# Kernel tuning notes

Hardware: AMD Instinct MI355X
Metric: run time of the kernel (lower is better)

Reference implementation:

```python
import jax, jax.numpy as jnp
import numpy as np

B, LATENT = 8192, 1024
NR, NC = 12, 12                      # nb_rows, nb_cols
H0, W0 = NR + 2, NC + 2              # 14x14 after reshape
EPS = 1e-5
SLOPE = 0.01                         # LeakyReLU default


def setup_inputs() -> dict:
    key = jax.random.key(0)
    ks = jax.random.split(key, 9)
    s = 0.05
    return {
        "x": jax.random.normal(ks[0], (B, LATENT), jnp.float32),
        "fc_w": jax.random.normal(ks[1], (H0 * W0 * 36, LATENT), jnp.float32) * s,
        "fc_b": jax.random.normal(ks[2], (H0 * W0 * 36,), jnp.float32) * s,
        "conv_w": jax.random.normal(ks[3], (16, 36, 2, 2), jnp.float32) * s,
        "conv_b": jax.random.normal(ks[4], (16,), jnp.float32) * s,
        "gamma": jnp.ones((16,), jnp.float32),
        "beta": jnp.zeros((16,), jnp.float32),
        # locally-connected weights: (out_ch, in_ch, Hout, Wout, k*k)
        "lw1": jax.random.normal(ks[5], (6, 16, H0 - 1, W0 - 1, 4), jnp.float32) * s,
        "lw2": jax.random.normal(ks[6], (1, 6, H0 - 2, W0 - 2, 4), jnp.float32) * s,
    }


def _leaky(x):
    return jnp.where(x >= 0, x, SLOPE * x)


def _local_conv2(x, w):
    # x: (B,C,H,W); w: (O,C,Ho,Wo,4) with k=2, stride 1, no padding
    Ho, Wo = w.shape[2], w.shape[3]
    patches = jnp.stack(
        [x[:, :, dy:dy + Ho, dx:dx + Wo] for dy in (0, 1) for dx in (0, 1)],
        axis=-1)  # (B,C,Ho,Wo,4)
    return jnp.einsum('bchwk,ochwk->bohw', patches, w)


def reference(x, fc_w, fc_b, conv_w, conv_b, gamma, beta, lw1, lw2):
    # fc -> view(B, H0, W0, 36) -> permute to NCHW
    h = x @ fc_w.T + fc_b
    h = h.reshape(B, H0, W0, 36).transpose(0, 3, 1, 2)  # (B,36,14,14)
    # Conv2d k=2 padding='same' (torch pads bottom/right for even kernels)
    h = jax.lax.conv_general_dilated(
        h, conv_w, window_strides=(1, 1), padding=((0, 1), (0, 1)),
        dimension_numbers=('NCHW', 'OIHW', 'NCHW')) + conv_b[None, :, None, None]
    h = _leaky(h)
    # BatchNorm2d (training mode: batch stats, biased var)
    mu = h.mean(axis=(0, 2, 3), keepdims=True)
    var = h.var(axis=(0, 2, 3), keepdims=True)
    h = (h - mu) * jax.lax.rsqrt(var + EPS)
    h = h * gamma[None, :, None, None] + beta[None, :, None, None]
    # locally-connected stack: 14x14 -> 13x13 -> 12x12
    h = _leaky(_local_conv2(h, lw1))
    return _local_conv2(h, lw2)  # (B,1,12,12)
```

## Files before the change

### kernel.cpp

```cpp
#include <hip/hip_runtime.h>


#define SLOPE 0.01f

typedef __bf16 bf16x8 __attribute__((ext_vector_type(8)));
typedef float f32x4 __attribute__((ext_vector_type(4)));

typedef const __attribute__((address_space(1))) void* gas_ptr;
typedef __attribute__((address_space(3))) void* las_ptr;

__device__ __forceinline__ void load16_to_lds(const void* g, void* l) {
  __builtin_amdgcn_global_load_lds((gas_ptr)g, (las_ptr)l, 16, 0, 0);
}

__device__ __forceinline__ unsigned short f2bf(float f) {
  union { float f; unsigned int u; } v; v.f = f;
  unsigned int r = v.u + 0x7FFFu + ((v.u >> 16) & 1u);
  return (unsigned short)(r >> 16);
}
__device__ __forceinline__ float bfbits2f(unsigned int bits16) {
  union { unsigned int u; float f; } v; v.u = bits16 << 16;
  return v.f;
}
__device__ __forceinline__ float leaky(float v) { return v >= 0.f ? v : SLOPE * v; }

__global__ void k_cast_x(const float* __restrict__ x, unsigned short* __restrict__ xb,
                         float* __restrict__ stats) {
  if (blockIdx.x == 0 && threadIdx.x < 32) stats[threadIdx.x] = 0.f;
  int gid = blockIdx.x * 256 + threadIdx.x;
  const float4* x4 = (const float4*)x;
  float4 a = x4[gid * 2], b = x4[gid * 2 + 1];
  union { unsigned short s[8]; uint4 v; } o;
  o.s[0] = f2bf(a.x); o.s[1] = f2bf(a.y); o.s[2] = f2bf(a.z); o.s[3] = f2bf(a.w);
  o.s[4] = f2bf(b.x); o.s[5] = f2bf(b.y); o.s[6] = f2bf(b.z); o.s[7] = f2bf(b.w);
  ((uint4*)xb)[gid] = o.v;
}

__global__ void k_fold(const float* __restrict__ fc_w, const float* __restrict__ fc_b,
                       const float* __restrict__ conv_w, const float* __restrict__ conv_b,
                       unsigned short* __restrict__ Wc, float* __restrict__ bc) {
  __shared__ float cw[2304];
  int blk = blockIdx.x, og = blockIdx.y, t = threadIdx.x;
  if (blk == 196) {
    if (og != 0) return;
    uint4 z = make_uint4(0, 0, 0, 0);
    uint4* dst = (uint4*)(Wc + 3136 * 1024);
    for (int i = t; i < 24576; i += 256) dst[i] = z;
    for (int i = 3136 + t; i < 3328; i += 256) bc[i] = 0.f;
    return;
  }
  for (int i = t; i < 2304; i += 256) cw[i] = conv_w[i];
  __syncthreads();
  int i0 = blk / 14, j0 = blk - (blk / 14) * 14;
  float acc[4][4];
#pragma unroll
  for (int o = 0; o < 4; o++)
#pragma unroll
    for (int q = 0; q < 4; q++) acc[o][q] = 0.f;
  for (int c = 0; c < 36; c++) {
#pragma unroll
    for (int dy = 0; dy < 2; dy++) {
      int ii = i0 + dy; if (ii > 13) continue;
#pragma unroll
      for (int dx = 0; dx < 2; dx++) {
        int jj = j0 + dx; if (jj > 13) continue;
        int row = (ii * 14 + jj) * 36 + c;
        float4 f = *(const float4*)(fc_w + row * 1024 + t * 4);
        int kk = dy * 2 + dx;
#pragma unroll
        for (int oo = 0; oo < 4; oo++) {
          int o = og * 4 + oo;
          float w = cw[(o * 36 + c) * 4 + kk];
          acc[oo][0] += w * f.x; acc[oo][1] += w * f.y;
          acc[oo][2] += w * f.z; acc[oo][3] += w * f.w;
        }
      }
    }
  }
#pragma unroll
  for (int oo = 0; oo < 4; oo++) {
    int o = og * 4 + oo;
    int n = o * 196 + i0 * 14 + j0;
    union { unsigned short s[4]; uint2 v; } u;
    u.s[0] = f2bf(acc[oo][0]); u.s[1] = f2bf(acc[oo][1]);
    u.s[2] = f2bf(acc[oo][2]); u.s[3] = f2bf(acc[oo][3]);
    *(uint2*)(Wc + n * 1024 + t * 4) = u.v;
  }
  if (og == 0 && t < 16) {
    int o = t;
    float b = conv_b[o];
    for (int c = 0; c < 36; c++)
      for (int dy = 0; dy < 2; dy++) {
        int ii = i0 + dy; if (ii > 13) continue;
        for (int dx = 0; dx < 2; dx++) {
          int jj = j0 + dx; if (jj > 13) continue;
          b += cw[(o * 36 + c) * 4 + dy * 2 + dx] * fc_b[(ii * 14 + jj) * 36 + c];
        }
      }
    bc[o * 196 + i0 * 14 + j0] = b;
  }
}

__global__ __launch_bounds__(512, 1) void k_gemm(const unsigned short* __restrict__ Xb,
                                                 const unsigned short* __restrict__ Wcb,
                                                 const float* __restrict__ bc,
                                                 unsigned short* __restrict__ h2,
                                                 float* __restrict__ stats) {
  __shared__ __align__(16) char lds[32768];
  __shared__ float red[8][4];
  const int t = threadIdx.x;
  const int w = t >> 6, lane = t & 63;
  const int quad = lane >> 4, l15 = lane & 15;
  const int d = blockIdx.x;
  const int xcd = d & 7, j = d >> 3;
  const int mblk = xcd * 4 + (j & 3);
  const int nblk = j >> 2;
  const int m0 = mblk * 256, n0 = nblk * 256;
  const int mrow = t & 255, tko = t >> 8;
  const unsigned short* ga = Xb + (m0 + mrow) * 1024 + tko * 8;
  const unsigned short* gb = Wcb + (n0 + mrow) * 1024 + tko * 8;
  char* lA = lds;
  char* lB = lds + 16384;
  const int wm = w >> 2, wn = w & 3;
  const int wm0 = wm * 128, wn0 = wn * 64;

  f32x4 acc[8][4];
#pragma unroll
  for (int a = 0; a < 8; a++)
#pragma unroll
    for (int b = 0; b < 4; b++) acc[a][b] = (f32x4){0.f, 0.f, 0.f, 0.f};

  for (int kb = 0; kb < 1024; kb += 32) {
    __syncthreads();
    load16_to_lds(ga + kb,      lA + t * 16);
    load16_to_lds(ga + kb + 16, lA + 8192 + t * 16);
    load16_to_lds(gb + kb,      lB + t * 16);
    load16_to_lds(gb + kb + 16, lB + 8192 + t * 16);
    __syncthreads();

    bf16x8 af[8], bfr[4];
#pragma unroll
    for (int mb = 0; mb < 8; mb++)
      af[mb] = *(const bf16x8*)(lA + quad * 4096 + (wm0 + mb * 16 + l15) * 16);
#pragma unroll
    for (int nb = 0; nb < 4; nb++)
      bfr[nb] = *(const bf16x8*)(lB + quad * 4096 + (wn0 + nb * 16 + l15) * 16);
#pragma unroll
    for (int mb = 0; mb < 8; mb++)
#pragma unroll
      for (int nb = 0; nb < 4; nb++)
        acc[mb][nb] = __builtin_amdgcn_mfma_f32_16x16x32_bf16(af[mb], bfr[nb], acc[mb][nb], 0, 0, 0);
  }

  const int chLo = (n0 + wn0) / 196;
  float ss0 = 0.f, ss1 = 0.f, sq0 = 0.f, sq1 = 0.f;
#pragma unroll
  for (int nb = 0; nb < 4; nb++) {
    int colb = n0 + wn0 + nb * 16;
    int col = colb + l15;
    float bias = bc[col];
    bool store_ok = colb < 3200;
    bool cnt = colb < 3136;
    bool hi = (col / 196) != chLo;
    float cs = 0.f, cq = 0.f;
#pragma unroll
    for (int mb = 0; mb < 8; mb++) {
#pragma unroll
      for (int r = 0; r < 4; r++) {
        int row = m0 + wm0 + mb * 16 + quad * 4 + r;
        float v = leaky(acc[mb][nb][r] + bias);
        if (store_ok) h2[row * 3200 + col] = f2bf(v);
        cs += v; cq += v * v;
      }
    }
    if (cnt) {
      if (hi) { ss1 += cs; sq1 += cq; } else { ss0 += cs; sq0 += cq; }
    }
  }
#pragma unroll
  for (int off = 1; off < 64; off <<= 1) {
    ss0 += __shfl_xor(ss0, off, 64);
    ss1 += __shfl_xor(ss1, off, 64);
    sq0 += __shfl_xor(sq0, off, 64);
    sq1 += __shfl_xor(sq1, off, 64);
  }
  if (lane == 0) { red[w][0] = ss0; red[w][1] = ss1; red[w][2] = sq0; red[w][3] = sq1; }
  __syncthreads();
  if (t == 0) {
#pragma unroll
    for (int w2 = 0; w2 < 8; w2++) {
      int cl = (n0 + (w2 & 3) * 64) / 196;
      if (cl < 16) {
        atomicAdd(&stats[cl], red[w2][0]);
        atomicAdd(&stats[16 + cl], red[w2][2]);
      }
      if (cl + 1 < 16) {
        atomicAdd(&stats[cl + 1], red[w2][1]);
        atomicAdd(&stats[16 + cl + 1], red[w2][3]);
      }
    }
  }
}

__global__ __launch_bounds__(256) void k_tail(const unsigned short* __restrict__ h2,
                                              const float* __restrict__ stats,
                                              const float* __restrict__ gamma,
                                              const float* __restrict__ beta,
                                              const float* __restrict__ lw1,
                                              const float* __restrict__ lw2,
                                              float* __restrict__ out) {
  __shared__ unsigned short h3[4 * 3138];
  __shared__ float h4[4 * 1015];
  __shared__ float sc[16], sh[16];
  int b0 = blockIdx.x * 4, t = threadIdx.x;
  if (t < 16) {
    const float inv = 1.f / 1605632.f;
    float mean = stats[t] * inv;
    float var = stats[16 + t] * inv - mean * mean;
    float rstd = rsqrtf(var + 1e-5f);
    float s = gamma[t] * rstd;
    sc[t] = s; sh[t] = beta[t] - mean * s;
  }
  __syncthreads();
  for (int i = t; i < 6272; i += 256) {
    int bb = i / 1568, q = i - bb * 1568;
    int n = q * 2, o = n / 196;
    unsigned int u = *(const unsigned int*)(h2 + (b0 + bb) * 3200 + n);
    float v0 = bfbits2f(u & 0xffffu) * sc[o] + sh[o];
    float v1 = bfbits2f(u >> 16) * sc[o] + sh[o];
    unsigned int pk = (unsigned int)f2bf(v0) | ((unsigned int)f2bf(v1) << 16);
    *(unsigned int*)(h3 + bb * 3138 + n) = pk;
  }
  __syncthreads();
  for (int u = t; u < 312; u += 256) {
    int bb = u & 3, rest = u >> 2;
    int o = rest / 13, y = rest - o * 13;
    float acc[13];
#pragma unroll
    for (int x = 0; x < 13; x++) acc[x] = 0.f;
    const unsigned short* hb = h3 + bb * 3138;
    for (int c = 0; c < 16; c++) {
      float r0[14], r1[14];
      const unsigned int* p0 = (const unsigned int*)(hb + c * 196 + y * 14);
      const unsigned int* p1 = (const unsigned int*)(hb + c * 196 + (y + 1) * 14);
#pragma unroll
      for (int q = 0; q < 7; q++) {
        unsigned int v0 = p0[q], v1 = p1[q];
        r0[2 * q] = bfbits2f(v0 & 0xffffu); r0[2 * q + 1] = bfbits2f(v0 >> 16);
        r1[2 * q] = bfbits2f(v1 & 0xffffu); r1[2 * q + 1] = bfbits2f(v1 >> 16);
      }
      const float4* wp4 = (const float4*)(lw1 + (((o * 16 + c) * 13 + y) * 13) * 4);
#pragma unroll
      for (int x = 0; x < 13; x++) {
        float4 wv = wp4[x];
        acc[x] += r0[x] * wv.x + r0[x + 1] * wv.y +
                  r1[x] * wv.z + r1[x + 1] * wv.w;
      }
    }
#pragma unroll
    for (int x = 0; x < 13; x++)
      h4[bb * 1015 + (o * 13 + y) * 13 + x] = leaky(acc[x]);
  }
  __syncthreads();
  for (int oi = t; oi < 576; oi += 256) {
    int pos = oi >> 2, bb = oi & 3;
    int y = pos / 12, x = pos - y * 12;
    float a = 0.f;
    const float* hp = h4 + bb * 1015;
    const float4* w4 = (const float4*)lw2;
#pragma unroll
    for (int c = 0; c < 6; c++) {
      float4 wv = w4[(c * 12 + y) * 12 + x];
      int hb = c * 169 + y * 13 + x;
      a += hp[hb] * wv.x + hp[hb + 1] * wv.y +
           hp[hb + 13] * wv.z + hp[hb + 14] * wv.w;
    }
    out[(b0 + bb) * 144 + pos] = a;
  }
}

extern "C" void kernel_launch(void* const* d_in, const int* in_sizes, int n_in,
                              void* d_out, int out_size, void* d_ws, size_t ws_size,
                              hipStream_t stream) {
  const float* x      = (const float*)d_in[0];
  const float* fc_w   = (const float*)d_in[1];
  const float* fc_b   = (const float*)d_in[2];
  const float* conv_w = (const float*)d_in[3];
  const float* conv_b = (const float*)d_in[4];
  const float* gamma  = (const float*)d_in[5];
  const float* beta   = (const float*)d_in[6];
  const float* lw1    = (const float*)d_in[7];
  const float* lw2    = (const float*)d_in[8];

  char* ws = (char*)d_ws;
  unsigned short* Xb    = (unsigned short*)(ws);
  unsigned short* Wc    = (unsigned short*)(ws + 16777216);
  float*          bc    = (float*)(ws + 23592960);
  float*          stats = (float*)(ws + 23606272);
  unsigned short* h2    = (unsigned short*)(ws + 23606400);

  k_cast_x<<<4096, 256, 0, stream>>>(x, Xb, stats);
  k_fold<<<dim3(197, 4), 256, 0, stream>>>(fc_w, fc_b, conv_w, conv_b, Wc, bc);
  k_gemm<<<416, 512, 0, stream>>>(Xb, Wc, bc, h2, stats);
  k_tail<<<2048, 256, 0, stream>>>(h2, stats, gamma, beta, lw1, lw2, (float*)d_out);
}
```

Measured before the change: 431.9 us.

## Double-buffer GEMM K-loop, reorganize weight folding, and share weights across rows in local conv

The bf16 GEMM now uses two 64-wide K stages in a 128KB LDS double buffer. The next stage is issued before computing the current one, which halves the barriers per K and overlaps global loads with MFMA. The weight-folding kernel now gives each thread one K column and all 16 output channels, with grid y split over K instead of output groups, which changes its memory access pattern. The first locally-connected layer now has each thread process two batch rows so each weight load is reused twice, at the cost of fewer active threads and more registers.

```diff
diff --git a/kernel.cpp b/kernel.cpp
--- a/kernel.cpp
+++ b/kernel.cpp
@@ -40,9 +40,9 @@
                        const float* __restrict__ conv_w, const float* __restrict__ conv_b,
                        unsigned short* __restrict__ Wc, float* __restrict__ bc) {
   __shared__ float cw[2304];
-  int blk = blockIdx.x, og = blockIdx.y, t = threadIdx.x;
+  int blk = blockIdx.x, kg = blockIdx.y, t = threadIdx.x;
   if (blk == 196) {
-    if (og != 0) return;
+    if (kg != 0) return;
     uint4 z = make_uint4(0, 0, 0, 0);
     uint4* dst = (uint4*)(Wc + 3136 * 1024);
     for (int i = t; i < 24576; i += 256) dst[i] = z;
@@ -52,11 +52,10 @@
   for (int i = t; i < 2304; i += 256) cw[i] = conv_w[i];
   __syncthreads();
   int i0 = blk / 14, j0 = blk - (blk / 14) * 14;
-  float acc[4][4];
-#pragma unroll
-  for (int o = 0; o < 4; o++)
-#pragma unroll
-    for (int q = 0; q < 4; q++) acc[o][q] = 0.f;
+  int kcol = kg * 256 + t;
+  float acc[16];
+#pragma unroll
+  for (int o = 0; o < 16; o++) acc[o] = 0.f;
   for (int c = 0; c < 36; c++) {
 #pragma unroll
     for (int dy = 0; dy < 2; dy++) {
@@ -65,28 +64,20 @@
       for (int dx = 0; dx < 2; dx++) {
         int jj = j0 + dx; if (jj > 13) continue;
         int row = (ii * 14 + jj) * 36 + c;
-        float4 f = *(const float4*)(fc_w + row * 1024 + t * 4);
+        float f = fc_w[row * 1024 + kcol];
         int kk = dy * 2 + dx;
 #pragma unroll
-        for (int oo = 0; oo < 4; oo++) {
-          int o = og * 4 + oo;
-          float w = cw[(o * 36 + c) * 4 + kk];
-          acc[oo][0] += w * f.x; acc[oo][1] += w * f.y;
-          acc[oo][2] += w * f.z; acc[oo][3] += w * f.w;
-        }
-      }
-    }
-  }
-#pragma unroll
-  for (int oo = 0; oo < 4; oo++) {
-    int o = og * 4 + oo;
+        for (int o = 0; o < 16; o++)
+          acc[o] += cw[(o * 36 + c) * 4 + kk] * f;
+      }
+    }
+  }
+#pragma unroll
+  for (int o = 0; o < 16; o++) {
     int n = o * 196 + i0 * 14 + j0;
-    union { unsigned short s[4]; uint2 v; } u;
-    u.s[0] = f2bf(acc[oo][0]); u.s[1] = f2bf(acc[oo][1]);
-    u.s[2] = f2bf(acc[oo][2]); u.s[3] = f2bf(acc[oo][3]);
-    *(uint2*)(Wc + n * 1024 + t * 4) = u.v;
-  }
-  if (og == 0 && t < 16) {
+    Wc[n * 1024 + kcol] = f2bf(acc[o]);
+  }
+  if (kg == 0 && t < 16) {
     int o = t;
     float b = conv_b[o];
     for (int c = 0; c < 36; c++)
@@ -106,7 +97,7 @@
                                                  const float* __restrict__ bc,
                                                  unsigned short* __restrict__ h2,
                                                  float* __restrict__ stats) {
-  __shared__ __align__(16) char lds[32768];
+  __shared__ __align__(16) char lds[131072];
   __shared__ float red[8][4];
   const int t = threadIdx.x;
   const int w = t >> 6, lane = t & 63;
@@ -119,8 +110,7 @@
   const int mrow = t & 255, tko = t >> 8;
   const unsigned short* ga = Xb + (m0 + mrow) * 1024 + tko * 8;
   const unsigned short* gb = Wcb + (n0 + mrow) * 1024 + tko * 8;
-  char* lA = lds;
-  char* lB = lds + 16384;
+  const int sbase = tko * 4096 + mrow * 16;
   const int wm = w >> 2, wn = w & 3;
   const int wm0 = wm * 128, wn0 = wn * 64;
 
@@ -130,27 +120,45 @@
 #pragma unroll
     for (int b = 0; b < 4; b++) acc[a][b] = (f32x4){0.f, 0.f, 0.f, 0.f};
 
-  for (int kb = 0; kb < 1024; kb += 32) {
+  auto stage = [&](int buf, int kb) {
+    char* sA = lds + buf * 65536;
+    char* sB = sA + 32768;
+#pragma unroll
+    for (int i = 0; i < 4; i++) {
+      load16_to_lds(ga + kb + i * 16, sA + i * 8192 + sbase);
+      load16_to_lds(gb + kb + i * 16, sB + i * 8192 + sbase);
+    }
+  };
+  auto compute = [&](int buf) {
+    char* lA = lds + buf * 65536;
+    char* lB = lA + 32768;
+#pragma unroll
+    for (int kk = 0; kk < 2; kk++) {
+      bf16x8 af[8], bfr[4];
+#pragma unroll
+      for (int mb = 0; mb < 8; mb++)
+        af[mb] = *(const bf16x8*)(lA + (kk * 4 + quad) * 4096 + (wm0 + mb * 16 + l15) * 16);
+#pragma unroll
+      for (int nb = 0; nb < 4; nb++)
+        bfr[nb] = *(const bf16x8*)(lB + (kk * 4 + quad) * 4096 + (wn0 + nb * 16 + l15) * 16);
+#pragma unroll
+      for (int mb = 0; mb < 8; mb++)
+#pragma unroll
+        for (int nb = 0; nb < 4; nb++)
+          acc[mb][nb] = __builtin_amdgcn_mfma_f32_16x16x32_bf16(af[mb], bfr[nb], acc[mb][nb], 0, 0, 0);
+    }
+  };
+
+  stage(0, 0);
+  __syncthreads();
+  int cur = 0;
+  for (int kb = 0; kb < 960; kb += 64) {
+    stage(cur ^ 1, kb + 64);
+    compute(cur);
     __syncthreads();
-    load16_to_lds(ga + kb,      lA + t * 16);
-    load16_to_lds(ga + kb + 16, lA + 8192 + t * 16);
-    load16_to_lds(gb + kb,      lB + t * 16);
-    load16_to_lds(gb + kb + 16, lB + 8192 + t * 16);
-    __syncthreads();
-
-    bf16x8 af[8], bfr[4];
-#pragma unroll
-    for (int mb = 0; mb < 8; mb++)
-      af[mb] = *(const bf16x8*)(lA + quad * 4096 + (wm0 + mb * 16 + l15) * 16);
-#pragma unroll
-    for (int nb = 0; nb < 4; nb++)
-      bfr[nb] = *(const bf16x8*)(lB + quad * 4096 + (wn0 + nb * 16 + l15) * 16);
-#pragma unroll
-    for (int mb = 0; mb < 8; mb++)
-#pragma unroll
-      for (int nb = 0; nb < 4; nb++)
-        acc[mb][nb] = __builtin_amdgcn_mfma_f32_16x16x32_bf16(af[mb], bfr[nb], acc[mb][nb], 0, 0, 0);
-  }
+    cur ^= 1;
+  }
+  compute(cur);
 
   const int chLo = (n0 + wn0) / 196;
   float ss0 = 0.f, ss1 = 0.f, sq0 = 0.f, sq1 = 0.f;
@@ -232,34 +240,42 @@
     *(unsigned int*)(h3 + bb * 3138 + n) = pk;
   }
   __syncthreads();
-  for (int u = t; u < 312; u += 256) {
-    int bb = u & 3, rest = u >> 2;
+  for (int u = t; u < 156; u += 256) {
+    int rp = u & 1, rest = u >> 1;
     int o = rest / 13, y = rest - o * 13;
-    float acc[13];
-#pragma unroll
-    for (int x = 0; x < 13; x++) acc[x] = 0.f;
-    const unsigned short* hb = h3 + bb * 3138;
+    int rA = 2 * rp, rB = 2 * rp + 1;
+    float acc0[13], acc1[13];
+#pragma unroll
+    for (int x = 0; x < 13; x++) { acc0[x] = 0.f; acc1[x] = 0.f; }
+    const unsigned short* hA = h3 + rA * 3138;
+    const unsigned short* hB = h3 + rB * 3138;
     for (int c = 0; c < 16; c++) {
-      float r0[14], r1[14];
-      const unsigned int* p0 = (const unsigned int*)(hb + c * 196 + y * 14);
-      const unsigned int* p1 = (const unsigned int*)(hb + c * 196 + (y + 1) * 14);
+      float a0[14], a1[14], e0[14], e1[14];
+      const unsigned int* pA0 = (const unsigned int*)(hA + c * 196 + y * 14);
+      const unsigned int* pA1 = (const unsigned int*)(hA + c * 196 + (y + 1) * 14);
+      const unsigned int* pB0 = (const unsigned int*)(hB + c * 196 + y * 14);
+      const unsigned int* pB1 = (const unsigned int*)(hB + c * 196 + (y + 1) * 14);
 #pragma unroll
       for (int q = 0; q < 7; q++) {
-        unsigned int v0 = p0[q], v1 = p1[q];
-        r0[2 * q] = bfbits2f(v0 & 0xffffu); r0[2 * q + 1] = bfbits2f(v0 >> 16);
-        r1[2 * q] = bfbits2f(v1 & 0xffffu); r1[2 * q + 1] = bfbits2f(v1 >> 16);
+        unsigned int vA0 = pA0[q], vA1 = pA1[q], vB0 = pB0[q], vB1 = pB1[q];
+        a0[2 * q] = bfbits2f(vA0 & 0xffffu); a0[2 * q + 1] = bfbits2f(vA0 >> 16);
+        a1[2 * q] = bfbits2f(vA1 & 0xffffu); a1[2 * q + 1] = bfbits2f(vA1 >> 16);
+        e0[2 * q] = bfbits2f(vB0 & 0xffffu); e0[2 * q + 1] = bfbits2f(vB0 >> 16);
+        e1[2 * q] = bfbits2f(vB1 & 0xffffu); e1[2 * q + 1] = bfbits2f(vB1 >> 16);
       }
       const float4* wp4 = (const float4*)(lw1 + (((o * 16 + c) * 13 + y) * 13) * 4);
 #pragma unroll
       for (int x = 0; x < 13; x++) {
         float4 wv = wp4[x];
-        acc[x] += r0[x] * wv.x + r0[x + 1] * wv.y +
-                  r1[x] * wv.z + r1[x + 1] * wv.w;
-      }
-    }
-#pragma unroll
-    for (int x = 0; x < 13; x++)
-      h4[bb * 1015 + (o * 13 + y) * 13 + x] = leaky(acc[x]);
+        acc0[x] += a0[x] * wv.x + a0[x + 1] * wv.y + a1[x] * wv.z + a1[x + 1] * wv.w;
+        acc1[x] += e0[x] * wv.x + e0[x + 1] * wv.y + e1[x] * wv.z + e1[x + 1] * wv.w;
+      }
+    }
+#pragma unroll
+    for (int x = 0; x < 13; x++) {
+      h4[rA * 1015 + (o * 13 + y) * 13 + x] = leaky(acc0[x]);
+      h4[rB * 1015 + (o * 13 + y) * 13 + x] = leaky(acc1[x]);
+    }
   }
   __syncthreads();
   for (int oi = t; oi < 576; oi += 256) {
```

New measurement: 447.2 us. +3.5%, slower.
